# Optimization experiments

Hardware: AMD Instinct MI355X
Metric: run time of the kernel (lower is better)

Reference implementation:

```python
import jax, jax.numpy as jnp
import numpy as np

N = 40000
E = 640000
D_IN = 128
D_OUT = 128
LN_EPS = 1e-5
LEAKY_ALPHA = 0.2


def setup_inputs() -> dict:
    key = jax.random.key(0)
    ks = jax.random.split(key, 8)
    x = jax.random.normal(ks[0], (N, D_IN), dtype=jnp.float32)
    edge_index = jax.random.randint(ks[1], (2, E), 0, N, dtype=jnp.int64)
    edge_weight = jax.random.uniform(ks[2], (E,), dtype=jnp.float32)
    # learned parameters (kaiming-uniform-ish init for weight)
    bound_w = np.sqrt(6.0 / D_IN) / np.sqrt(1.0 + 5.0)
    weight = jax.random.uniform(ks[3], (D_IN, D_OUT), minval=-bound_w, maxval=bound_w, dtype=jnp.float32)
    adaptive_weight = jax.random.uniform(ks[4], (1,), dtype=jnp.float32)
    bound_b = 1.0 / np.sqrt(D_IN)
    bias = jax.random.uniform(ks[5], (D_OUT,), minval=-bound_b, maxval=bound_b, dtype=jnp.float32)
    ln_gamma = jnp.ones((D_OUT,), dtype=jnp.float32)
    ln_beta = jnp.zeros((D_OUT,), dtype=jnp.float32)
    return {"x": x, "edge_index": edge_index, "edge_weight": edge_weight,
            "weight": weight, "adaptive_weight": adaptive_weight, "bias": bias,
            "ln_gamma": ln_gamma, "ln_beta": ln_beta}


def reference(x, edge_index, edge_weight, weight, adaptive_weight, bias, ln_gamma, ln_beta):
    n = x.shape[0]
    out = x @ weight  # [N, D_OUT]
    row, col = edge_index[0], edge_index[1]
    aew = edge_weight * jax.nn.sigmoid(adaptive_weight[0])  # [E]
    # degree via scatter_add over row
    deg = jax.ops.segment_sum(aew, row, num_segments=n)  # [N]
    deg_inv_sqrt = jnp.where(deg > 0, deg ** -0.5, 0.0)
    norm = deg_inv_sqrt[row] * aew * deg_inv_sqrt[col]  # [E]
    # gather-scale-scatter propagate
    out = jax.ops.segment_sum(out[col] * norm[:, None], row, num_segments=n)  # [N, D_OUT]
    out = out + bias
    # LayerNorm over feature dim
    mu = jnp.mean(out, axis=-1, keepdims=True)
    var = jnp.mean((out - mu) ** 2, axis=-1, keepdims=True)
    out = (out - mu) * jax.lax.rsqrt(var + LN_EPS) * ln_gamma + ln_beta
    # LeakyReLU
    out = jnp.where(out >= 0, out, LEAKY_ALPHA * out)
    return out
```

## Files before the change

kernel.cpp:

```cpp
#include <hip/hip_runtime.h>
#include <hip/hip_bf16.h>
#include <math.h>

#define N_NODES 40000
#define E_EDGES 640000
#define D 128
#define LN_EPS 1e-5f
#define LEAKY 0.2f
#define NB 157

#define BM 32
__global__ __launch_bounds__(256) void k_gemm(const float* __restrict__ x,
                                              const float* __restrict__ w,
                                              __hip_bfloat16* __restrict__ outb,
                                              int* __restrict__ cnt) {
    int gid = blockIdx.x * 256 + threadIdx.x;
    if (gid < N_NODES) cnt[gid] = 0;

    __shared__ float ws[128 * 128];
    __shared__ float xs[BM * 128];
    int t = threadIdx.x;

    const float4* w4 = (const float4*)w;
    float4* ws4 = (float4*)ws;
#pragma unroll
    for (int i = 0; i < 16; i++) ws4[t + i * 256] = w4[t + i * 256];

    int row0 = blockIdx.x * BM;
    const float4* x4 = (const float4*)(x + (size_t)row0 * D);
    float4* xs4 = (float4*)xs;
#pragma unroll
    for (int i = 0; i < 4; i++) xs4[t + i * 256] = x4[t + i * 256];

    __syncthreads();

    int c0 = (t & 31) * 4;
    int r0 = (t >> 5) * 4;
    float acc[4][4] = {};
#pragma unroll 4
    for (int k = 0; k < 128; k++) {
        float4 wv = *(const float4*)&ws[k * 128 + c0];
        float x0 = xs[(r0 + 0) * 128 + k];
        float x1 = xs[(r0 + 1) * 128 + k];
        float x2 = xs[(r0 + 2) * 128 + k];
        float x3 = xs[(r0 + 3) * 128 + k];
        acc[0][0] += x0 * wv.x; acc[0][1] += x0 * wv.y; acc[0][2] += x0 * wv.z; acc[0][3] += x0 * wv.w;
        acc[1][0] += x1 * wv.x; acc[1][1] += x1 * wv.y; acc[1][2] += x1 * wv.z; acc[1][3] += x1 * wv.w;
        acc[2][0] += x2 * wv.x; acc[2][1] += x2 * wv.y; acc[2][2] += x2 * wv.z; acc[2][3] += x2 * wv.w;
        acc[3][0] += x3 * wv.x; acc[3][1] += x3 * wv.y; acc[3][2] += x3 * wv.z; acc[3][3] += x3 * wv.w;
    }
#pragma unroll
    for (int i = 0; i < 4; i++) {
        int row = row0 + r0 + i;
        __hip_bfloat162 p0 = __float22bfloat162_rn(make_float2(acc[i][0], acc[i][1]));
        __hip_bfloat162 p1 = __float22bfloat162_rn(make_float2(acc[i][2], acc[i][3]));
        uint2 pk;
        pk.x = *(unsigned int*)&p0;
        pk.y = *(unsigned int*)&p1;
        *(uint2*)&outb[(size_t)row * D + c0] = pk;
    }
}

__global__ __launch_bounds__(256) void k_cnt(const int* __restrict__ ei,
                                             int* __restrict__ cnt,
                                             int* __restrict__ rank) {
    int e = blockIdx.x * 256 + threadIdx.x;
    if (e >= E_EDGES) return;
    rank[e] = atomicAdd(&cnt[ei[e]], 1);
}

__global__ __launch_bounds__(256) void k_scanA(const int* __restrict__ cnt,
                                               int* __restrict__ bsum) {
    __shared__ int red[256];
    int t = threadIdx.x;
    int i = blockIdx.x * 256 + t;
    red[t] = (i < N_NODES) ? cnt[i] : 0;
    __syncthreads();
    for (int off = 128; off > 0; off >>= 1) {
        if (t < off) red[t] += red[t + off];
        __syncthreads();
    }
    if (t == 0) bsum[blockIdx.x] = red[0];
}

__global__ __launch_bounds__(256) void k_scanB(const int* __restrict__ bsum,
                                               int* __restrict__ boff,
                                               int* __restrict__ rowstart) {
    __shared__ int s[256];
    int t = threadIdx.x;
    int v = (t < NB) ? bsum[t] : 0;
    s[t] = v;
    __syncthreads();
    for (int off = 1; off < 256; off <<= 1) {
        int u = (t >= off) ? s[t - off] : 0;
        __syncthreads();
        s[t] += u;
        __syncthreads();
    }
    if (t < NB) boff[t] = s[t] - v;
    if (t == 0) rowstart[N_NODES] = E_EDGES;
}

__global__ __launch_bounds__(256) void k_scanC(const int* __restrict__ cnt,
                                               const int* __restrict__ boff,
                                               int* __restrict__ rowstart) {
    __shared__ int s[256];
    int t = threadIdx.x;
    int i = blockIdx.x * 256 + t;
    int v = (i < N_NODES) ? cnt[i] : 0;
    s[t] = v;
    __syncthreads();
    for (int off = 1; off < 256; off <<= 1) {
        int u = (t >= off) ? s[t - off] : 0;
        __syncthreads();
        s[t] += u;
        __syncthreads();
    }
    if (i < N_NODES) rowstart[i] = boff[blockIdx.x] + s[t] - v;
}

__global__ __launch_bounds__(256) void k_scat(const int* __restrict__ ei,
                                              const float* __restrict__ ew,
                                              const float* __restrict__ aw,
                                              const int* __restrict__ rowstart,
                                              const int* __restrict__ rank,
                                              float2* __restrict__ srec) {
    int e = blockIdx.x * 256 + threadIdx.x;
    if (e >= E_EDGES) return;
    float sig = 1.f / (1.f + __expf(-aw[0]));
    int r = ei[e];
    int c = ei[E_EDGES + e];
    int slot = rowstart[r] + rank[e];
    srec[slot] = make_float2(__int_as_float(c), ew[e] * sig);
}

__global__ __launch_bounds__(256) void k_degdis(const int* __restrict__ rowstart,
                                                const float2* __restrict__ srec,
                                                float* __restrict__ dis) {
    int i = blockIdx.x * 256 + threadIdx.x;
    if (i >= N_NODES) return;
    int s = rowstart[i];
    int e = rowstart[i + 1];
    float d = 0.f;
    for (int j = s; j < e; j++) d += srec[j].y;
    dis[i] = (d > 0.f) ? rsqrtf(d) : 0.f;
}

__global__ __launch_bounds__(256) void k_agg(const int* __restrict__ rowstart,
                                             const float2* __restrict__ srec,
                                             const __hip_bfloat162* __restrict__ lin2,
                                             const float* __restrict__ dis,
                                             const float* __restrict__ bias,
                                             const float* __restrict__ gamma,
                                             const float* __restrict__ beta,
                                             float* __restrict__ out) {
    int w = (blockIdx.x * 256 + threadIdx.x) >> 6;
    int lane = threadIdx.x & 63;
    if (w >= N_NODES) return;
    int s = __builtin_amdgcn_readfirstlane(rowstart[w]);
    int e = __builtin_amdgcn_readfirstlane(rowstart[w + 1]);
    float dr = dis[w];

    float2 acc = make_float2(0.f, 0.f);
    int i = s;
    for (; i + 4 <= e; i += 4) {
        float2 r0 = srec[i];
        float2 r1 = srec[i + 1];
        float2 r2 = srec[i + 2];
        float2 r3 = srec[i + 3];
        int c0 = __float_as_int(r0.x);
        int c1 = __float_as_int(r1.x);
        int c2 = __float_as_int(r2.x);
        int c3 = __float_as_int(r3.x);
        __hip_bfloat162 t0 = lin2[(size_t)c0 * 64 + lane];
        __hip_bfloat162 t1 = lin2[(size_t)c1 * 64 + lane];
        __hip_bfloat162 t2 = lin2[(size_t)c2 * 64 + lane];
        __hip_bfloat162 t3 = lin2[(size_t)c3 * 64 + lane];
        float v0 = r0.y * dis[c0];
        float v1 = r1.y * dis[c1];
        float v2 = r2.y * dis[c2];
        float v3 = r3.y * dis[c3];
        float2 f0 = __bfloat1622float2(t0);
        float2 f1 = __bfloat1622float2(t1);
        float2 f2 = __bfloat1622float2(t2);
        float2 f3 = __bfloat1622float2(t3);
        acc.x += f0.x * v0; acc.y += f0.y * v0;
        acc.x += f1.x * v1; acc.y += f1.y * v1;
        acc.x += f2.x * v2; acc.y += f2.y * v2;
        acc.x += f3.x * v3; acc.y += f3.y * v3;
    }
    for (; i < e; i++) {
        float2 rec = srec[i];
        int c = __float_as_int(rec.x);
        float v = rec.y * dis[c];
        __hip_bfloat162 t = lin2[(size_t)c * 64 + lane];
        float2 tf = __bfloat1622float2(t);
        acc.x += tf.x * v;
        acc.y += tf.y * v;
    }
    acc.x *= dr; acc.y *= dr;

    float2 b = *(const float2*)&bias[lane * 2];
    acc.x += b.x; acc.y += b.y;

    float sm = acc.x + acc.y;
#pragma unroll
    for (int m = 1; m < 64; m <<= 1) sm += __shfl_xor(sm, m);
    float mu = sm * (1.f / 128.f);

    float dx = acc.x - mu, dy = acc.y - mu;
    float q = dx * dx + dy * dy;
#pragma unroll
    for (int m = 1; m < 64; m <<= 1) q += __shfl_xor(q, m);
    float rstd = rsqrtf(q * (1.f / 128.f) + LN_EPS);

    float2 g  = *(const float2*)&gamma[lane * 2];
    float2 be = *(const float2*)&beta[lane * 2];
    float y0 = dx * rstd * g.x + be.x;
    float y1 = dy * rstd * g.y + be.y;
    y0 = (y0 >= 0.f) ? y0 : LEAKY * y0;
    y1 = (y1 >= 0.f) ? y1 : LEAKY * y1;
    *(float2*)&out[(size_t)w * D + lane * 2] = make_float2(y0, y1);
}

extern "C" void kernel_launch(void* const* d_in, const int* in_sizes, int n_in,
                              void* d_out, int out_size, void* d_ws, size_t ws_size,
                              hipStream_t stream) {
    const float* x      = (const float*)d_in[0];
    const int*   ei     = (const int*)d_in[1];
    const float* ew     = (const float*)d_in[2];
    const float* w      = (const float*)d_in[3];
    const float* aw     = (const float*)d_in[4];
    const float* bias   = (const float*)d_in[5];
    const float* gamma  = (const float*)d_in[6];
    const float* beta   = (const float*)d_in[7];
    float* out = (float*)d_out;

    char* p = (char*)d_ws;
    __hip_bfloat16* out_lin = (__hip_bfloat16*)p; p += (size_t)N_NODES * D * 2;
    float* dis      = (float*)p;            p += N_NODES * 4;
    int*   cnt      = (int*)p;              p += N_NODES * 4;
    int*   rowstart = (int*)p;              p += (N_NODES + 1) * 4;
    int*   rank     = (int*)p;              p += (size_t)E_EDGES * 4;
    int*   bsum     = (int*)p;              p += NB * 4;
    int*   boff     = (int*)p;              p += NB * 4;
    float2* srec    = (float2*)((((uintptr_t)p) + 15) & ~(uintptr_t)15);

    k_gemm<<<N_NODES / BM, 256, 0, stream>>>(x, w, out_lin, cnt);
    k_cnt<<<(E_EDGES + 255) / 256, 256, 0, stream>>>(ei, cnt, rank);
    k_scanA<<<NB, 256, 0, stream>>>(cnt, bsum);
    k_scanB<<<1, 256, 0, stream>>>(bsum, boff, rowstart);
    k_scanC<<<NB, 256, 0, stream>>>(cnt, boff, rowstart);
    k_scat<<<(E_EDGES + 255) / 256, 256, 0, stream>>>(ei, ew, aw, rowstart, rank, srec);
    k_degdis<<<NB, 256, 0, stream>>>(rowstart, srec, dis);
    k_agg<<<(N_NODES + 3) / 4, 256, 0, stream>>>(rowstart, srec,
                                                 (const __hip_bfloat162*)out_lin, dis,
                                                 bias, gamma, beta, out);
}
```

Before: 194.2 us.

## Fuse edge counting into GEMM, parallelize degree sum, unroll aggregation by 8

The row-count atomics move into the GEMM kernel, with each of the 1250 blocks handling 512 edges, and zeroing gets its own small kernel. This removes a separate launch and lets the atomic latency overlap with the GEMM loads. The degree kernel now uses 4 threads per row with shuffle reductions instead of one serial thread. The aggregation loop gains an 8-wide unrolled gather to keep more loads in flight, at the cost of higher register pressure.

```diff
diff --git a/kernel.cpp b/kernel.cpp
--- a/kernel.cpp
+++ b/kernel.cpp
@@ -9,24 +9,37 @@
 #define LEAKY 0.2f
 #define NB 157
 
+__global__ __launch_bounds__(256) void k_zero(int* __restrict__ cnt) {
+    int i = blockIdx.x * 256 + threadIdx.x;
+    if (i < N_NODES) cnt[i] = 0;
+}
+
 #define BM 32
-__global__ __launch_bounds__(256) void k_gemm(const float* __restrict__ x,
-                                              const float* __restrict__ w,
-                                              __hip_bfloat16* __restrict__ outb,
-                                              int* __restrict__ cnt) {
-    int gid = blockIdx.x * 256 + threadIdx.x;
-    if (gid < N_NODES) cnt[gid] = 0;
+__global__ __launch_bounds__(256) void k_gemmcnt(const float* __restrict__ x,
+                                                 const float* __restrict__ w,
+                                                 const int* __restrict__ ei,
+                                                 __hip_bfloat16* __restrict__ outb,
+                                                 int* __restrict__ cnt,
+                                                 int* __restrict__ rank) {
+    int t = threadIdx.x;
+    int blk = blockIdx.x;
+
+    int e0 = blk * 512 + t;
+    int e1 = e0 + 256;
+    int er0 = ei[e0];
+    int er1 = ei[e1];
+    int k0 = atomicAdd(&cnt[er0], 1);
+    int k1 = atomicAdd(&cnt[er1], 1);
 
     __shared__ float ws[128 * 128];
     __shared__ float xs[BM * 128];
-    int t = threadIdx.x;
 
     const float4* w4 = (const float4*)w;
     float4* ws4 = (float4*)ws;
 #pragma unroll
     for (int i = 0; i < 16; i++) ws4[t + i * 256] = w4[t + i * 256];
 
-    int row0 = blockIdx.x * BM;
+    int row0 = blk * BM;
     const float4* x4 = (const float4*)(x + (size_t)row0 * D);
     float4* xs4 = (float4*)xs;
 #pragma unroll
@@ -59,14 +72,9 @@
         pk.y = *(unsigned int*)&p1;
         *(uint2*)&outb[(size_t)row * D + c0] = pk;
     }
-}
-
-__global__ __launch_bounds__(256) void k_cnt(const int* __restrict__ ei,
-                                             int* __restrict__ cnt,
-                                             int* __restrict__ rank) {
-    int e = blockIdx.x * 256 + threadIdx.x;
-    if (e >= E_EDGES) return;
-    rank[e] = atomicAdd(&cnt[ei[e]], 1);
+
+    rank[e0] = k0;
+    rank[e1] = k1;
 }
 
 __global__ __launch_bounds__(256) void k_scanA(const int* __restrict__ cnt,
@@ -137,13 +145,17 @@
 __global__ __launch_bounds__(256) void k_degdis(const int* __restrict__ rowstart,
                                                 const float2* __restrict__ srec,
                                                 float* __restrict__ dis) {
-    int i = blockIdx.x * 256 + threadIdx.x;
-    if (i >= N_NODES) return;
-    int s = rowstart[i];
-    int e = rowstart[i + 1];
+    int t = threadIdx.x;
+    int row = (blockIdx.x * 256 + t) >> 2;
+    int sub = t & 3;
+    if (row >= N_NODES) return;
+    int s = rowstart[row];
+    int e = rowstart[row + 1];
     float d = 0.f;
-    for (int j = s; j < e; j++) d += srec[j].y;
-    dis[i] = (d > 0.f) ? rsqrtf(d) : 0.f;
+    for (int j = s + sub; j < e; j += 4) d += srec[j].y;
+    d += __shfl_xor(d, 1);
+    d += __shfl_xor(d, 2);
+    if (sub == 0) dis[row] = (d > 0.f) ? rsqrtf(d) : 0.f;
 }
 
 __global__ __launch_bounds__(256) void k_agg(const int* __restrict__ rowstart,
@@ -163,6 +175,26 @@
 
     float2 acc = make_float2(0.f, 0.f);
     int i = s;
+    for (; i + 8 <= e; i += 8) {
+        float2 rr[8];
+#pragma unroll
+        for (int u = 0; u < 8; u++) rr[u] = srec[i + u];
+        int cc[8];
+#pragma unroll
+        for (int u = 0; u < 8; u++) cc[u] = __float_as_int(rr[u].x);
+        __hip_bfloat162 tt[8];
+#pragma unroll
+        for (int u = 0; u < 8; u++) tt[u] = lin2[(size_t)cc[u] * 64 + lane];
+        float vv[8];
+#pragma unroll
+        for (int u = 0; u < 8; u++) vv[u] = rr[u].y * dis[cc[u]];
+#pragma unroll
+        for (int u = 0; u < 8; u++) {
+            float2 f = __bfloat1622float2(tt[u]);
+            acc.x += f.x * vv[u];
+            acc.y += f.y * vv[u];
+        }
+    }
     for (; i + 4 <= e; i += 4) {
         float2 r0 = srec[i];
         float2 r1 = srec[i + 1];
@@ -246,13 +278,13 @@
     int*   boff     = (int*)p;              p += NB * 4;
     float2* srec    = (float2*)((((uintptr_t)p) + 15) & ~(uintptr_t)15);
 
-    k_gemm<<<N_NODES / BM, 256, 0, stream>>>(x, w, out_lin, cnt);
-    k_cnt<<<(E_EDGES + 255) / 256, 256, 0, stream>>>(ei, cnt, rank);
+    k_zero<<<NB, 256, 0, stream>>>(cnt);
+    k_gemmcnt<<<N_NODES / BM, 256, 0, stream>>>(x, w, ei, out_lin, cnt, rank);
     k_scanA<<<NB, 256, 0, stream>>>(cnt, bsum);
     k_scanB<<<1, 256, 0, stream>>>(bsum, boff, rowstart);
     k_scanC<<<NB, 256, 0, stream>>>(cnt, boff, rowstart);
     k_scat<<<(E_EDGES + 255) / 256, 256, 0, stream>>>(ei, ew, aw, rowstart, rank, srec);
-    k_degdis<<<NB, 256, 0, stream>>>(rowstart, srec, dis);
+    k_degdis<<<(N_NODES * 4 + 255) / 256, 256, 0, stream>>>(rowstart, srec, dis);
     k_agg<<<(N_NODES + 3) / 4, 256, 0, stream>>>(rowstart, srec,
                                                  (const __hip_bfloat162*)out_lin, dis,
                                                  bias, gamma, beta, out);
```

Result: faster. 178.0 us (-8.3%).
